# Kernel tuning notes

Measured on AMD Instinct MI355X. Metric: run time of the kernel, lower is better.

## Reference

```python
import jax, jax.numpy as jnp
import numpy as np

N, H, W, C = 2, 96, 96, 256
HEADS, P = 8, 25
DH = C // HEADS
HID = int(C * 4.0)


def _ln(x, g, b):
    m = jnp.mean(x, axis=-1, keepdims=True)
    v = jnp.var(x, axis=-1, keepdims=True)
    return (x - m) / jnp.sqrt(v + 1e-5) * g + b


def _deform_sample(value, loc, h, w):
    # value: (n, heads, h*w, dh); loc: (n, Lq, heads, P, 2) normalized to [0,1] (x,y)
    # Bilinear sampling with align_corners=False and zero padding, as in
    # grid_sample used by MSDeformAttn.
    n = value.shape[0]
    gx = loc[..., 0] * w - 0.5
    gy = loc[..., 1] * h - 0.5
    x0 = jnp.floor(gx)
    y0 = jnp.floor(gy)
    fx = gx - x0
    fy = gy - y0
    out = jnp.zeros((n, HEADS, gx.shape[1] * P, DH), dtype=value.dtype)
    for dx, dy in ((0, 0), (1, 0), (0, 1), (1, 1)):
        xi = x0 + dx
        yi = y0 + dy
        wgt = (fx if dx else 1.0 - fx) * (fy if dy else 1.0 - fy)
        valid = ((xi >= 0) & (xi <= w - 1) & (yi >= 0) & (yi <= h - 1)).astype(value.dtype)
        xi_c = jnp.clip(xi, 0, w - 1).astype(jnp.int32)
        yi_c = jnp.clip(yi, 0, h - 1).astype(jnp.int32)
        idx = yi_c * w + xi_c                                   # (n, Lq, heads, P)
        idx = jnp.transpose(idx, (0, 2, 1, 3)).reshape(n, HEADS, -1)
        g = jnp.take_along_axis(value, idx[..., None], axis=2)  # (n, heads, Lq*P, dh)
        wv = jnp.transpose(wgt * valid, (0, 2, 1, 3)).reshape(n, HEADS, -1, 1)
        out = out + g * wv
    return out


def setup_inputs() -> dict:
    key = jax.random.key(0)
    ks = jax.random.split(key, 20)
    s = 0.02
    inp = {
        'x': jax.random.normal(ks[0], (N, H, W, C), jnp.float32),
        'ref_points': jax.random.uniform(ks[1], (N, H * W, 1, 2), jnp.float32),
        'spatial_shapes': jnp.array([[H, W]], dtype=jnp.int32),
        'level_start_index': jnp.zeros((1,), dtype=jnp.int32),
        'ln1_g': jnp.ones((C,), jnp.float32),
        'ln1_b': jnp.zeros((C,), jnp.float32),
        'w_off': jax.random.normal(ks[2], (C, HEADS * P * 2), jnp.float32) * s,
        'b_off': jax.random.normal(ks[3], (HEADS * P * 2,), jnp.float32) * s,
        'w_attn': jax.random.normal(ks[4], (C, HEADS * P), jnp.float32) * s,
        'b_attn': jax.random.normal(ks[5], (HEADS * P,), jnp.float32) * s,
        'w_val': jax.random.normal(ks[6], (C, C), jnp.float32) * s,
        'b_val': jnp.zeros((C,), jnp.float32),
        'w_out': jax.random.normal(ks[7], (C, C), jnp.float32) * s,
        'b_out': jnp.zeros((C,), jnp.float32),
        'ln2_g': jnp.ones((C,), jnp.float32),
        'ln2_b': jnp.zeros((C,), jnp.float32),
        'w_fc1': jax.random.normal(ks[8], (C, HID), jnp.float32) * s,
        'b_fc1': jnp.zeros((HID,), jnp.float32),
        'w_fc2': jax.random.normal(ks[9], (HID, C), jnp.float32) * s,
        'b_fc2': jnp.zeros((C,), jnp.float32),
    }
    return inp


def reference(x, ref_points, spatial_shapes, level_start_index,
              ln1_g, ln1_b, w_off, b_off, w_attn, b_attn,
              w_val, b_val, w_out, b_out, ln2_g, ln2_b,
              w_fc1, b_fc1, w_fc2, b_fc2):
    n, h, w, c = x.shape
    lq = h * w
    shortcut = x
    # pre-norm + flatten to query
    q = _ln(x, ln1_g, ln1_b).reshape(n, lq, c)
    # MSDeformAttn (n_levels = 1)
    value = (q @ w_val + b_val).reshape(n, lq, HEADS, DH).transpose(0, 2, 1, 3)
    off = (q @ w_off + b_off).reshape(n, lq, HEADS, P, 2)
    aw = jax.nn.softmax((q @ w_attn + b_attn).reshape(n, lq, HEADS, P), axis=-1)
    norm = jnp.array([w, h], dtype=x.dtype)          # offsets normalized by (W, H)
    ref = ref_points[:, :, 0, :]                     # (n, Lq, 2)
    loc = ref[:, :, None, None, :] + off / norm      # (n, Lq, heads, P, 2)
    sampled = _deform_sample(value, loc, h, w).reshape(n, HEADS, lq, P, DH)
    attn = jnp.einsum('nqhp,nhqpd->nqhd', aw, sampled).reshape(n, lq, c)
    attn = attn @ w_out + b_out
    x1 = shortcut + attn.reshape(n, h, w, c)
    # MLP block
    y = _ln(x1, ln2_g, ln2_b)
    y = jax.nn.gelu(y @ w_fc1 + b_fc1, approximate=False) @ w_fc2 + b_fc2
    return x1 + y
```

## Files before the change

### kernel.cpp

```cpp
#include <hip/hip_runtime.h>
#include <hip/hip_bf16.h>
#include <math.h>

typedef __hip_bfloat16 bf16;
typedef __attribute__((ext_vector_type(8))) short short8;
typedef __attribute__((ext_vector_type(4))) float f32x4;

#define NB 2
#define HH 96
#define WW 96
#define CC 256
#define NHEADS 8
#define PP 25
#define DHH 32
#define HIDN 1024
#define LQ (HH*WW)
#define TT (NB*LQ)
#define NVC 896
#define TB 4

__device__ __forceinline__ float b2f(bf16 v){ return __bfloat162float(v); }
__device__ __forceinline__ bf16  f2b(float v){ return __float2bfloat16(v); }
__device__ __forceinline__ float lo_bf(unsigned u){ return __uint_as_float(u << 16); }
__device__ __forceinline__ float hi_bf(unsigned u){ return __uint_as_float(u & 0xffff0000u); }

__device__ __forceinline__ void gl2lds16(const void* g, void* l) {
    __builtin_amdgcn_global_load_lds(
        (const __attribute__((address_space(1))) unsigned int*)g,
        (__attribute__((address_space(3))) unsigned int*)l, 16, 0, 0);
}

__global__ __launch_bounds__(256) void fused_pre(const float* __restrict__ x,
                                                 const float* __restrict__ ln1_g,
                                                 const float* __restrict__ ln1_b,
                                                 bf16* __restrict__ q,
                                                 const float* __restrict__ w_val,
                                                 const float* __restrict__ w_off,
                                                 const float* __restrict__ w_attn,
                                                 const float* __restrict__ w_fc1,
                                                 const float* __restrict__ w_fc2,
                                                 const float* __restrict__ w_out,
                                                 const float* __restrict__ b_val,
                                                 const float* __restrict__ b_off,
                                                 const float* __restrict__ b_attn,
                                                 bf16* __restrict__ wvcT,
                                                 bf16* __restrict__ wfc1T,
                                                 bf16* __restrict__ wfc2T,
                                                 bf16* __restrict__ woutT,
                                                 float* __restrict__ bvc)
{
    const int bid = blockIdx.x;
    if (bid < 4608) {
        const int t = bid*4 + (threadIdx.x >> 6);
        const int l = threadIdx.x & 63;
        const float4 v = *(const float4*)(x + (size_t)t*CC + l*4);
        float s  = v.x + v.y + v.z + v.w;
        float s2 = v.x*v.x + v.y*v.y + v.z*v.z + v.w*v.w;
        #pragma unroll
        for (int m = 1; m < 64; m <<= 1) { s += __shfl_xor(s, m); s2 += __shfl_xor(s2, m); }
        const float mean = s * (1.f/CC);
        const float var  = s2 * (1.f/CC) - mean*mean;
        const float rs   = 1.f / sqrtf(var + 1e-5f);
        const float4 gg = *(const float4*)(ln1_g + l*4);
        const float4 bb = *(const float4*)(ln1_b + l*4);
        bf16 o[4];
        o[0] = f2b((v.x-mean)*rs*gg.x + bb.x);
        o[1] = f2b((v.y-mean)*rs*gg.y + bb.y);
        o[2] = f2b((v.z-mean)*rs*gg.z + bb.z);
        o[3] = f2b((v.w-mean)*rs*gg.w + bb.w);
        *(uint2*)(q + (size_t)t*CC + l*4) = *(uint2*)o;
    } else {
        const int idx = (bid - 4608)*256 + threadIdx.x;
        if (idx < 229376) {
            int n = idx >> 8, k = idx & 255;
            float v = (n < 256) ? w_val[(size_t)k*256 + n]
                    : (n < 656) ? w_off[(size_t)k*400 + (n-256)]
                    : (n < 856) ? w_attn[(size_t)k*200 + (n-656)] : 0.f;
            wvcT[idx] = f2b(v);
        } else if (idx < 491520) {
            int j = idx - 229376; int n = j >> 8, k = j & 255;
            wfc1T[j] = f2b(w_fc1[(size_t)k*1024 + n]);
        } else if (idx < 753664) {
            int j = idx - 491520; int n = j >> 10, k = j & 1023;
            wfc2T[j] = f2b(w_fc2[(size_t)k*256 + n]);
        } else if (idx < 819200) {
            int j = idx - 753664; int n = j >> 8, k = j & 255;
            woutT[j] = f2b(w_out[(size_t)k*256 + n]);
        }
        if (idx < NVC)
            bvc[idx] = (idx < 256) ? b_val[idx]
                     : (idx < 656) ? b_off[idx-256]
                     : (idx < 856) ? b_attn[idx-656] : 0.f;
    }
}

__global__ __launch_bounds__(256) void ln_kernel(const float* __restrict__ x,
                                                 const float* __restrict__ g,
                                                 const float* __restrict__ b,
                                                 bf16* __restrict__ out)
{
    const int t = blockIdx.x*4 + (threadIdx.x >> 6);
    const int l = threadIdx.x & 63;
    const float4 v = *(const float4*)(x + (size_t)t*CC + l*4);
    float s  = v.x + v.y + v.z + v.w;
    float s2 = v.x*v.x + v.y*v.y + v.z*v.z + v.w*v.w;
    #pragma unroll
    for (int m = 1; m < 64; m <<= 1) { s += __shfl_xor(s, m); s2 += __shfl_xor(s2, m); }
    const float mean = s * (1.f/CC);
    const float var  = s2 * (1.f/CC) - mean*mean;
    const float rs   = 1.f / sqrtf(var + 1e-5f);
    const float4 gg = *(const float4*)(g + l*4);
    const float4 bb = *(const float4*)(b + l*4);
    bf16 o[4];
    o[0] = f2b((v.x-mean)*rs*gg.x + bb.x);
    o[1] = f2b((v.y-mean)*rs*gg.y + bb.y);
    o[2] = f2b((v.z-mean)*rs*gg.z + bb.z);
    o[3] = f2b((v.w-mean)*rs*gg.w + bb.w);
    *(uint2*)(out + (size_t)t*CC + l*4) = *(uint2*)o;
}

template<int EPI, int K, int N, int TM>
__global__ __launch_bounds__(256) void mfma_gemm(const bf16* __restrict__ A,
                                                 const bf16* __restrict__ Bt,
                                                 const float* __restrict__ bias,
                                                 void* __restrict__ outv,
                                                 const float* __restrict__ resid,
                                                 bf16* __restrict__ val_d)
{
    constexpr int AR  = TM/8;
    constexpr int TR  = AR + 16;
    constexpr int RPW = TR/4;
    constexpr int NJ  = (TM==128) ? 4 : 2;
    __shared__ short As[TM*64];
    __shared__ short Bs[128*64];
    const int tid = threadIdx.x;
    const int w = tid >> 6, l = tid & 63;
    const int bm = blockIdx.x, bn = blockIdx.y;

    const bf16* sbase[RPW];
    short*      lbase[RPW];
    {
        const int lrow = l >> 3;
        const int q    = (l & 7) ^ lrow;
        #pragma unroll
        for (int j = 0; j < RPW; j++) {
            int r = w*RPW + j;
            bool isA = r < AR;
            int rr = isA ? r : r - AR;
            int row = rr*8 + lrow;
            size_t grow = (size_t)(isA ? (bm*TM + row) : (bn*128 + row));
            sbase[j] = (isA ? A : Bt) + grow*K + q*8;
            lbase[j] = (isA ? As : Bs) + rr*512;
        }
    }

    const int mbase = (TM==128) ? 64*(w >> 1) : 0;
    const int nbase = (TM==128) ? 64*(w & 1)  : 32*w;

    int aoff[2][4], boff[2][NJ];
    #pragma unroll
    for (int s = 0; s < 2; s++) {
        const int q = s*4 + (l >> 4);
        #pragma unroll
        for (int i = 0; i < 4; i++) {
            int m = mbase + i*16 + (l & 15);
            aoff[s][i] = (m*8 + (q ^ (m & 7))) * 8;
        }
        #pragma unroll
        for (int j = 0; j < NJ; j++) {
            int n = nbase + j*16 + (l & 15);
            boff[s][j] = (n*8 + (q ^ (n & 7))) * 8;
        }
    }

    f32x4 acc[4][NJ];
    #pragma unroll
    for (int i = 0; i < 4; i++)
        #pragma unroll
        for (int j = 0; j < NJ; j++)
            acc[i][j] = (f32x4){0.f, 0.f, 0.f, 0.f};

    for (int k0 = 0; k0 < K; k0 += 64) {
        #pragma unroll
        for (int j = 0; j < RPW; j++)
            gl2lds16(sbase[j] + k0, lbase[j]);
        __syncthreads();
        #pragma unroll
        for (int s = 0; s < 2; s++) {
            short8 af[4], bfr[NJ];
            #pragma unroll
            for (int i = 0; i < 4; i++)  af[i]  = *(const short8*)(As + aoff[s][i]);
            #pragma unroll
            for (int j = 0; j < NJ; j++) bfr[j] = *(const short8*)(Bs + boff[s][j]);
            #pragma unroll
            for (int i = 0; i < 4; i++)
                #pragma unroll
                for (int j = 0; j < NJ; j++)
                    acc[i][j] = __builtin_amdgcn_mfma_f32_16x16x32_bf16(af[i], bfr[j], acc[i][j], 0, 0, 0);
        }
        __syncthreads();
    }

    const int row0 = bm*TM + mbase + (l >> 4)*4;
    const int col0 = bn*128 + nbase + (l & 15);
    #pragma unroll
    for (int i = 0; i < 4; i++) {
        #pragma unroll
        for (int j = 0; j < NJ; j++) {
            const int col = col0 + j*16;
            const float bs = bias[col];
            #pragma unroll
            for (int r = 0; r < 4; r++) {
                const int row = row0 + i*16 + r;
                float v = acc[i][j][r] + bs;
                size_t o = (size_t)row * N + col;
                if (EPI == 0) {
                    ((bf16*)outv)[o] = f2b(v);
                } else if (EPI == 2) {
                    ((bf16*)outv)[o] = f2b(0.5f * v * (1.f + erff(v * 0.70710678118654752f)));
                } else if (EPI == 3) {
                    ((float*)outv)[o] = v + resid[o];
                } else {
                    if (col < 256) val_d[(size_t)row*CC + col] = f2b(v);
                    else           ((bf16*)outv)[o] = f2b(v);
                }
            }
        }
    }
}

struct __align__(16) Tap { _Float16 w[4]; unsigned short i[4]; };

__global__ __launch_bounds__(128) void sample_kernel(const bf16* __restrict__ vc,
                                                     const bf16* __restrict__ val_d,
                                                     const float* __restrict__ refp,
                                                     bf16* __restrict__ samp)
{
    __shared__ Tap taps[TB*200];
    const int b = blockIdx.x;
    const int xcd = b & 7, sub = b >> 3;
    const int tbase = (xcd >> 2)*LQ + ((xcd & 3)*576 + sub)*TB;
    const int tid = threadIdx.x;

    {
        const int pair = tid >> 2;
        const int j    = tid & 3;
        const int tl   = pair >> 3;
        const int h    = pair & 7;
        const int t    = tbase + tl;
        const bf16* row = vc + (size_t)t*NVC;

        float lg[7];
        #pragma unroll
        for (int k = 0; k < 7; k++) {
            int p = j + 4*k;
            lg[k] = (p < PP) ? b2f(row[656 + h*25 + p]) : -1e30f;
        }
        float m = lg[0];
        #pragma unroll
        for (int k = 1; k < 7; k++) m = fmaxf(m, lg[k]);
        m = fmaxf(m, __shfl_xor(m, 1));
        m = fmaxf(m, __shfl_xor(m, 2));
        float s = 0.f;
        float ex[7];
        #pragma unroll
        for (int k = 0; k < 7; k++) {
            ex[k] = (j + 4*k < PP) ? expf(lg[k] - m) : 0.f;
            s += ex[k];
        }
        s += __shfl_xor(s, 1);
        s += __shfl_xor(s, 2);
        const float inv = 1.f / s;

        const float rx96 = refp[(size_t)t*2 + 0]*96.f - 0.5f;
        const float ry96 = refp[(size_t)t*2 + 1]*96.f - 0.5f;
        const unsigned* offp = (const unsigned*)(row + 256 + h*50);

        #pragma unroll
        for (int k = 0; k < 7; k++) {
            const int p = j + 4*k;
            if (p >= PP) break;
            const float a = ex[k] * inv;
            const unsigned uo = offp[p];
            const float gx = rx96 + lo_bf(uo);
            const float gy = ry96 + hi_bf(uo);
            const float x0f = floorf(gx), y0f = floorf(gy);
            const float fx = gx - x0f, fy = gy - y0f;
            const int ix = (int)x0f, iy = (int)y0f;
            Tap tp;
            #pragma unroll
            for (int d = 0; d < 4; d++) {
                const int dx = d & 1, dy = d >> 1;
                const int xi = ix + dx, yi = iy + dy;
                const bool valid = (xi >= 0) & (xi <= WW-1) & (yi >= 0) & (yi <= HH-1);
                const int xc = min(max(xi, 0), WW-1);
                const int yc = min(max(yi, 0), HH-1);
                tp.i[d] = (unsigned short)(yc*WW + xc);
                tp.w[d] = (_Float16)(valid ? a * (dx ? fx : 1.f-fx) * (dy ? fy : 1.f-fy) : 0.f);
            }
            taps[tl*200 + h*25 + p] = tp;
        }
    }
    __syncthreads();

    const int wv_ = tid >> 6, l = tid & 63;
    const int tl  = wv_*2 + (l >> 5);
    const int r   = l & 31;
    const int h   = r >> 2, oct = r & 3;
    const int c0  = h*DHH + oct*8;
    const int t   = tbase + tl;
    const int n   = (t >= LQ) ? 1 : 0;
    const bf16* pv = val_d + (size_t)n*LQ*CC + c0;
    const int pib = tl*200 + h*25;

    float acc[8] = {0.f,0.f,0.f,0.f,0.f,0.f,0.f,0.f};
    for (int p = 0; p < PP; p++) {
        const uint4 tv = *((const uint4*)taps + (pib + p));
        const _Float16* wp_ = (const _Float16*)&tv;
        const unsigned short* ip_ = (const unsigned short*)&tv + 4;
        #pragma unroll
        for (int d = 0; d < 4; d++) {
            const float wt = (float)wp_[d];
            const uint4 vv = *(const uint4*)(pv + (size_t)ip_[d]*CC);
            acc[0] += wt*lo_bf(vv.x); acc[1] += wt*hi_bf(vv.x);
            acc[2] += wt*lo_bf(vv.y); acc[3] += wt*hi_bf(vv.y);
            acc[4] += wt*lo_bf(vv.z); acc[5] += wt*hi_bf(vv.z);
            acc[6] += wt*lo_bf(vv.w); acc[7] += wt*hi_bf(vv.w);
        }
    }
    bf16 o[8];
    #pragma unroll
    for (int j2 = 0; j2 < 8; j2++) o[j2] = f2b(acc[j2]);
    *(uint4*)(samp + (size_t)t*CC + c0) = *(uint4*)o;
}

extern "C" void kernel_launch(void* const* d_in, const int* in_sizes, int n_in,
                              void* d_out, int out_size, void* d_ws, size_t ws_size,
                              hipStream_t stream)
{
    const float* x      = (const float*)d_in[0];
    const float* refp   = (const float*)d_in[1];
    const float* ln1_g  = (const float*)d_in[4];
    const float* ln1_b  = (const float*)d_in[5];
    const float* w_off  = (const float*)d_in[6];
    const float* b_off  = (const float*)d_in[7];
    const float* w_attn = (const float*)d_in[8];
    const float* b_attn = (const float*)d_in[9];
    const float* w_val  = (const float*)d_in[10];
    const float* b_val  = (const float*)d_in[11];
    const float* w_out  = (const float*)d_in[12];
    const float* b_out  = (const float*)d_in[13];
    const float* ln2_g  = (const float*)d_in[14];
    const float* ln2_b  = (const float*)d_in[15];
    const float* w_fc1  = (const float*)d_in[16];
    const float* b_fc1  = (const float*)d_in[17];
    const float* w_fc2  = (const float*)d_in[18];
    const float* b_fc2  = (const float*)d_in[19];

    char* wsb = (char*)d_ws;
    bf16*  q     = (bf16*)(wsb + 0);
    bf16*  vc    = (bf16*)(wsb + 9437184);
    bf16*  samp  = (bf16*)(wsb + 42467328);
    float* x1    = (float*)(wsb + 51904512);
    bf16*  wvcT  = (bf16*)(wsb + 70778880);
    bf16*  wfc1T = (bf16*)(wsb + 71237632);
    bf16*  wfc2T = (bf16*)(wsb + 71761920);
    bf16*  woutT = (bf16*)(wsb + 72286208);
    float* bvc   = (float*)(wsb + 72417280);
    bf16*  val_d = (bf16*)(wsb + 72420864);
    bf16*  hid   = (bf16*)(wsb + 0);
    bf16*  y0    = samp;

    if (ws_size < 81858048) return;

    const dim3 blk(256);
    fused_pre<<<dim3(7808), blk, 0, stream>>>(x, ln1_g, ln1_b, q,
                                              w_val, w_off, w_attn, w_fc1, w_fc2, w_out,
                                              b_val, b_off, b_attn,
                                              wvcT, wfc1T, wfc2T, woutT, bvc);
    mfma_gemm<4,256,NVC,128><<<dim3(TT/128, NVC/128), blk, 0, stream>>>(q, wvcT, bvc, (void*)vc, nullptr, val_d);
    sample_kernel<<<dim3(TT/TB), dim3(128), 0, stream>>>(vc, val_d, refp, samp);
    mfma_gemm<3,256,CC,64><<<dim3(TT/64, CC/128), blk, 0, stream>>>(samp, woutT, b_out, (void*)x1, x, nullptr);
    ln_kernel<<<dim3(TT/4), blk, 0, stream>>>(x1, ln2_g, ln2_b, y0);
    mfma_gemm<2,256,HIDN,128><<<dim3(TT/128, HIDN/128), blk, 0, stream>>>(y0, wfc1T, b_fc1, (void*)hid, nullptr, nullptr);
    mfma_gemm<3,HIDN,CC,64><<<dim3(TT/64, CC/128), blk, 0, stream>>>(hid, wfc2T, b_fc2, d_out, x1, nullptr);
}
```

Measured before the change: 243.5 us.

## Store values as fp16 and accumulate sampling with packed half2 FMAs

The value tensor is now written as fp16 instead of bf16, and the deformable sampling kernel accumulates with packed __hfma2 on half2 pairs instead of unpacking to fp32 and doing scalar FMAs. This halves the ALU instruction count in the gather loop. The sampling block also grows to 8 tokens and 256 threads, with the XCD-based tile mapping adjusted to match. The cost is lower accumulation precision (fp16 over 100 taps) and a possible overflow or accuracy risk.

New measurement: 245.5 us. About the same (+0.8%).

```diff
diff --git a/kernel.cpp b/kernel.cpp
--- a/kernel.cpp
+++ b/kernel.cpp
@@ -1,5 +1,6 @@
 #include <hip/hip_runtime.h>
 #include <hip/hip_bf16.h>
+#include <hip/hip_fp16.h>
 #include <math.h>
 
 typedef __hip_bfloat16 bf16;
@@ -17,7 +18,7 @@
 #define LQ (HH*WW)
 #define TT (NB*LQ)
 #define NVC 896
-#define TB 4
+#define TB 8
 
 __device__ __forceinline__ float b2f(bf16 v){ return __bfloat162float(v); }
 __device__ __forceinline__ bf16  f2b(float v){ return __float2bfloat16(v); }
@@ -125,7 +126,7 @@
                                                  const float* __restrict__ bias,
                                                  void* __restrict__ outv,
                                                  const float* __restrict__ resid,
-                                                 bf16* __restrict__ val_d)
+                                                 __half* __restrict__ val_d)
 {
     constexpr int AR  = TM/8;
     constexpr int TR  = AR + 16;
@@ -221,7 +222,7 @@
                 } else if (EPI == 3) {
                     ((float*)outv)[o] = v + resid[o];
                 } else {
-                    if (col < 256) val_d[(size_t)row*CC + col] = f2b(v);
+                    if (col < 256) val_d[(size_t)row*CC + col] = __float2half(v);
                     else           ((bf16*)outv)[o] = f2b(v);
                 }
             }
@@ -231,15 +232,15 @@
 
 struct __align__(16) Tap { _Float16 w[4]; unsigned short i[4]; };
 
-__global__ __launch_bounds__(128) void sample_kernel(const bf16* __restrict__ vc,
-                                                     const bf16* __restrict__ val_d,
+__global__ __launch_bounds__(256) void sample_kernel(const bf16* __restrict__ vc,
+                                                     const __half* __restrict__ val_d,
                                                      const float* __restrict__ refp,
                                                      bf16* __restrict__ samp)
 {
     __shared__ Tap taps[TB*200];
     const int b = blockIdx.x;
     const int xcd = b & 7, sub = b >> 3;
-    const int tbase = (xcd >> 2)*LQ + ((xcd & 3)*576 + sub)*TB;
+    const int tbase = (xcd >> 2)*LQ + ((xcd & 3)*288 + sub)*TB;
     const int tid = threadIdx.x;
 
     {
@@ -310,27 +311,34 @@
     const int c0  = h*DHH + oct*8;
     const int t   = tbase + tl;
     const int n   = (t >= LQ) ? 1 : 0;
-    const bf16* pv = val_d + (size_t)n*LQ*CC + c0;
+    const __half* pv = val_d + (size_t)n*LQ*CC + c0;
     const int pib = tl*200 + h*25;
 
-    float acc[8] = {0.f,0.f,0.f,0.f,0.f,0.f,0.f,0.f};
+    __half2 acc0 = __float2half2_rn(0.f);
+    __half2 acc1 = __float2half2_rn(0.f);
+    __half2 acc2 = __float2half2_rn(0.f);
+    __half2 acc3 = __float2half2_rn(0.f);
     for (int p = 0; p < PP; p++) {
         const uint4 tv = *((const uint4*)taps + (pib + p));
-        const _Float16* wp_ = (const _Float16*)&tv;
+        const __half* wp_ = (const __half*)&tv;
         const unsigned short* ip_ = (const unsigned short*)&tv + 4;
         #pragma unroll
         for (int d = 0; d < 4; d++) {
-            const float wt = (float)wp_[d];
-            const uint4 vv = *(const uint4*)(pv + (size_t)ip_[d]*CC);
-            acc[0] += wt*lo_bf(vv.x); acc[1] += wt*hi_bf(vv.x);
-            acc[2] += wt*lo_bf(vv.y); acc[3] += wt*hi_bf(vv.y);
-            acc[4] += wt*lo_bf(vv.z); acc[5] += wt*hi_bf(vv.z);
-            acc[6] += wt*lo_bf(vv.w); acc[7] += wt*hi_bf(vv.w);
+            const __half2 w2 = __half2half2(wp_[d]);
+            const __half2* vp = (const __half2*)(pv + (size_t)ip_[d]*CC);
+            const uint4 raw = *(const uint4*)vp;
+            const __half2* v2 = (const __half2*)&raw;
+            acc0 = __hfma2(w2, v2[0], acc0);
+            acc1 = __hfma2(w2, v2[1], acc1);
+            acc2 = __hfma2(w2, v2[2], acc2);
+            acc3 = __hfma2(w2, v2[3], acc3);
         }
     }
     bf16 o[8];
-    #pragma unroll
-    for (int j2 = 0; j2 < 8; j2++) o[j2] = f2b(acc[j2]);
+    o[0] = f2b(__low2float(acc0)); o[1] = f2b(__high2float(acc0));
+    o[2] = f2b(__low2float(acc1)); o[3] = f2b(__high2float(acc1));
+    o[4] = f2b(__low2float(acc2)); o[5] = f2b(__high2float(acc2));
+    o[6] = f2b(__low2float(acc3)); o[7] = f2b(__high2float(acc3));
     *(uint4*)(samp + (size_t)t*CC + c0) = *(uint4*)o;
 }
 
@@ -358,18 +366,18 @@
     const float* b_fc2  = (const float*)d_in[19];
 
     char* wsb = (char*)d_ws;
-    bf16*  q     = (bf16*)(wsb + 0);
-    bf16*  vc    = (bf16*)(wsb + 9437184);
-    bf16*  samp  = (bf16*)(wsb + 42467328);
-    float* x1    = (float*)(wsb + 51904512);
-    bf16*  wvcT  = (bf16*)(wsb + 70778880);
-    bf16*  wfc1T = (bf16*)(wsb + 71237632);
-    bf16*  wfc2T = (bf16*)(wsb + 71761920);
-    bf16*  woutT = (bf16*)(wsb + 72286208);
-    float* bvc   = (float*)(wsb + 72417280);
-    bf16*  val_d = (bf16*)(wsb + 72420864);
-    bf16*  hid   = (bf16*)(wsb + 0);
-    bf16*  y0    = samp;
+    bf16*   q     = (bf16*)(wsb + 0);
+    bf16*   vc    = (bf16*)(wsb + 9437184);
+    bf16*   samp  = (bf16*)(wsb + 42467328);
+    float*  x1    = (float*)(wsb + 51904512);
+    bf16*   wvcT  = (bf16*)(wsb + 70778880);
+    bf16*   wfc1T = (bf16*)(wsb + 71237632);
+    bf16*   wfc2T = (bf16*)(wsb + 71761920);
+    bf16*   woutT = (bf16*)(wsb + 72286208);
+    float*  bvc   = (float*)(wsb + 72417280);
+    __half* val_d = (__half*)(wsb + 72420864);
+    bf16*   hid   = (bf16*)(wsb + 0);
+    bf16*   y0    = samp;
 
     if (ws_size < 81858048) return;
 
@@ -379,7 +387,7 @@
                                               b_val, b_off, b_attn,
                                               wvcT, wfc1T, wfc2T, woutT, bvc);
     mfma_gemm<4,256,NVC,128><<<dim3(TT/128, NVC/128), blk, 0, stream>>>(q, wvcT, bvc, (void*)vc, nullptr, val_d);
-    sample_kernel<<<dim3(TT/TB), dim3(128), 0, stream>>>(vc, val_d, refp, samp);
+    sample_kernel<<<dim3(TT/TB), blk, 0, stream>>>(vc, val_d, refp, samp);
     mfma_gemm<3,256,CC,64><<<dim3(TT/64, CC/128), blk, 0, stream>>>(samp, woutT, b_out, (void*)x1, x, nullptr);
     ln_kernel<<<dim3(TT/4), blk, 0, stream>>>(x1, ln2_g, ln2_b, y0);
     mfma_gemm<2,256,HIDN,128><<<dim3(TT/128, HIDN/128), blk, 0, stream>>>(y0, wfc1T, b_fc1, (void*)hid, nullptr, nullptr);
```
